# Kernel optimization log

Measured on AMD Instinct MI355X. Metric: run time of the kernel, lower is better.

Reference implementation:

```python
import jax, jax.numpy as jnp
import numpy as np

B, L, D, H = 1024, 128, 768, 256
EPS = 1e-5  # torch BatchNorm1d default eps


def _masked_mean(x, lens):
    # x: [B, L, D], lens: [B] int -> mean over first lens[i] rows per sample
    mask = (jnp.arange(x.shape[1])[None, :] < lens[:, None]).astype(x.dtype)  # [B, L]
    return jnp.einsum('bld,bl->bd', x, mask) / lens[:, None].astype(x.dtype)


def _batchnorm_train(x, gamma, beta):
    # training-mode BN: batch mean and biased variance
    mu = jnp.mean(x, axis=0)
    var = jnp.mean((x - mu) ** 2, axis=0)
    return gamma * (x - mu) / jnp.sqrt(var + EPS) + beta


def setup_inputs() -> dict:
    key = jax.random.key(0)
    ks = jax.random.split(key, 12)
    user_features = jax.random.normal(ks[0], (B, L, D), jnp.float32)
    hashtag_features = jax.random.normal(ks[1], (B, L, D), jnp.float32)
    user_lens = jax.random.randint(ks[2], (B,), 1, L + 1, jnp.int32)
    hashtag_lens = jax.random.randint(ks[3], (B,), 1, L + 1, jnp.int32)
    def lin(k, fan_out, fan_in):
        bound = 1.0 / np.sqrt(fan_in)
        kw, kb = jax.random.split(k)
        w = jax.random.uniform(kw, (fan_out, fan_in), jnp.float32, -bound, bound)
        b = jax.random.uniform(kb, (fan_out,), jnp.float32, -bound, bound)
        return w, b
    fc1_w, fc1_b = lin(ks[4], D, 2 * D)
    fc2_w, fc2_b = lin(ks[5], H, D)
    fc3_w, fc3_b = lin(ks[6], 1, H)
    bn1_g = jnp.ones((D,), jnp.float32)
    bn1_b = jnp.zeros((D,), jnp.float32)
    bn2_g = jnp.ones((H,), jnp.float32)
    bn2_b = jnp.zeros((H,), jnp.float32)
    return {
        'user_features': user_features, 'hashtag_features': hashtag_features,
        'user_lens': user_lens, 'hashtag_lens': hashtag_lens,
        'fc1_w': fc1_w, 'fc1_b': fc1_b, 'bn1_g': bn1_g, 'bn1_b': bn1_b,
        'fc2_w': fc2_w, 'fc2_b': fc2_b, 'bn2_g': bn2_g, 'bn2_b': bn2_b,
        'fc3_w': fc3_w, 'fc3_b': fc3_b,
    }


def reference(user_features, hashtag_features, user_lens, hashtag_lens,
              fc1_w, fc1_b, bn1_g, bn1_b, fc2_w, fc2_b, bn2_g, bn2_b,
              fc3_w, fc3_b):
    # fused ragged mean pooling (replaces per-sample python loop)
    u = _masked_mean(user_features, user_lens)       # [B, D]
    h = _masked_mean(hashtag_features, hashtag_lens)  # [B, D]
    x = jnp.concatenate([u, h], axis=1)               # [B, 2D]
    x = jax.nn.relu(_batchnorm_train(x @ fc1_w.T + fc1_b, bn1_g, bn1_b))
    x = jax.nn.relu(_batchnorm_train(x @ fc2_w.T + fc2_b, bn2_g, bn2_b))
    out = jax.nn.sigmoid(x @ fc3_w.T + fc3_b)          # [B, 1]
    return out
```

## Files before the change

kernel.cpp:

```cpp
#include <hip/hip_runtime.h>
#include <cstdint>
#include <cstddef>

#define BATCH 1024
#define SEQL  128
#define DIM   768
#define HID   256
#define KIN1  1536
#define BN_EPS 1e-5f

typedef unsigned short u16;
typedef __attribute__((ext_vector_type(8))) short short8;
typedef __attribute__((ext_vector_type(4))) float f32x4;

__device__ __forceinline__ u16 f2bf(float f) {
  uint32_t u = __float_as_uint(f);
  return (u16)((u + 0x7fffu + ((u >> 16) & 1u)) >> 16);
}
__device__ __forceinline__ f32x4 ntl(const f32x4* p) { return __builtin_nontemporal_load(p); }
__device__ __forceinline__ float kred(float v) {
  v += __shfl_xor(v, 16);
  v += __shfl_xor(v, 32);
  return v;
}

#define POOL_BLK 4096
#define PREP_BLK 448
#define NW1Q (DIM * KIN1 / 4)
#define NWQ  (NW1Q + HID * DIM / 4)

__global__ __launch_bounds__(96) void pool_prep_kernel(
    const float* __restrict__ uf, const float* __restrict__ hf,
    const int* __restrict__ ul, const int* __restrict__ hl,
    const float* __restrict__ w1, const float* __restrict__ w2,
    u16* __restrict__ xb, u16* __restrict__ w1b, u16* __restrict__ w2b) {
  const int id = blockIdx.x;
  const int t = threadIdx.x;
  if (id < POOL_BLK) {
    const int b = id >> 2;
    const int which = (id >> 1) & 1;
    const int half = id & 1;
    const f32x4* src = (const f32x4*)((which ? hf : uf) + (size_t)b * (SEQL * DIM)) + half * 96;
    const int len = which ? hl[b] : ul[b];
    f32x4 a0 = (f32x4){0.f, 0.f, 0.f, 0.f}, a1 = a0, a2 = a0, a3 = a0;
    int l = 0;
    for (; l + 8 <= len; l += 8) {
      f32x4 v0 = ntl(src + (size_t)(l + 0) * 192 + t);
      f32x4 v1 = ntl(src + (size_t)(l + 1) * 192 + t);
      f32x4 v2 = ntl(src + (size_t)(l + 2) * 192 + t);
      f32x4 v3 = ntl(src + (size_t)(l + 3) * 192 + t);
      f32x4 v4 = ntl(src + (size_t)(l + 4) * 192 + t);
      f32x4 v5 = ntl(src + (size_t)(l + 5) * 192 + t);
      f32x4 v6 = ntl(src + (size_t)(l + 6) * 192 + t);
      f32x4 v7 = ntl(src + (size_t)(l + 7) * 192 + t);
      a0 += v0; a1 += v1; a2 += v2; a3 += v3;
      a0 += v4; a1 += v5; a2 += v6; a3 += v7;
    }
    for (; l < len; ++l) a0 += ntl(src + (size_t)l * 192 + t);
    a0 += a1; a2 += a3; a0 += a2;
    const float s = 1.f / (float)len;
    ushort4 o = make_ushort4(f2bf(a0[0] * s), f2bf(a0[1] * s), f2bf(a0[2] * s), f2bf(a0[3] * s));
    *(ushort4*)(xb + (size_t)b * KIN1 + which * DIM + half * 384 + t * 4) = o;
  } else {
    const int j = id - POOL_BLK;
    const int base = j * 96 + t;
#pragma unroll
    for (int s = 0; s < 8; ++s) {
      const int i = base + s * (PREP_BLK * 96);
      if (i < NW1Q) {
        f32x4 v = ((const f32x4*)w1)[i];
        ((ushort4*)w1b)[i] = make_ushort4(f2bf(v[0]), f2bf(v[1]), f2bf(v[2]), f2bf(v[3]));
      } else {
        const int i2 = i - NW1Q;
        f32x4 v = ((const f32x4*)w2)[i2];
        ((ushort4*)w2b)[i2] = make_ushort4(f2bf(v[0]), f2bf(v[1]), f2bf(v[2]), f2bf(v[3]));
      }
    }
  }
}

#define LDT 72

__global__ __launch_bounds__(256) void gemm1_kernel(
    const u16* __restrict__ A, const u16* __restrict__ W,
    const float* __restrict__ bias, float* __restrict__ y, float* __restrict__ p1) {
  __shared__ u16 lA[2][64 * LDT];
  __shared__ u16 lB[2][64 * LDT];
  __shared__ float red[2][64][2];
  const int K = KIN1, N = DIM;
  const int tid = threadIdx.x, lane = tid & 63, wv = tid >> 6;
  const int wr = wv >> 1, wc = wv & 1;
  const int r16 = lane & 15, kgrp = lane >> 4;
  const int d = blockIdx.x;
  const int g = d & 7, j = d >> 3;
  const int bm = (g >> 1) * 4 + (j & 3);
  const int bn = (g & 1) * 6 + (j >> 2);
  const int sr = tid >> 3, sc8 = (tid & 7) * 8;

  f32x4 acc[2][2];
#pragma unroll
  for (int mi = 0; mi < 2; ++mi)
#pragma unroll
    for (int ni = 0; ni < 2; ++ni) acc[mi][ni] = (f32x4){0.f, 0.f, 0.f, 0.f};

  const u16* Ab = A + (size_t)bm * 64 * K;
  const u16* Wb = W + (size_t)bn * 64 * K;

  uint4 ra0, ra1, rb0, rb1;
#define G1_LOAD(k0)                                              \
  ra0 = *(const uint4*)(Ab + (size_t)sr * K + (k0) + sc8);       \
  ra1 = *(const uint4*)(Ab + (size_t)(sr + 32) * K + (k0) + sc8);\
  rb0 = *(const uint4*)(Wb + (size_t)sr * K + (k0) + sc8);       \
  rb1 = *(const uint4*)(Wb + (size_t)(sr + 32) * K + (k0) + sc8);
#define G1_WRITE(buf)                                \
  *(uint4*)(lA[buf] + sr * LDT + sc8) = ra0;         \
  *(uint4*)(lA[buf] + (sr + 32) * LDT + sc8) = ra1;  \
  *(uint4*)(lB[buf] + sr * LDT + sc8) = rb0;         \
  *(uint4*)(lB[buf] + (sr + 32) * LDT + sc8) = rb1;

  G1_LOAD(0)
  G1_WRITE(0)
  __syncthreads();
  const int nk = K / 64;
  for (int ti = 0; ti < nk; ++ti) {
    const int cur = ti & 1;
    const bool more = (ti + 1 < nk);
    if (more) { G1_LOAD((ti + 1) * 64) }
#pragma unroll
    for (int kk = 0; kk < 2; ++kk) {
      const int koff = (kk * 4 + kgrp) * 8;
      short8 af0 = *(const short8*)(lA[cur] + (wr * 32 + r16) * LDT + koff);
      short8 af1 = *(const short8*)(lA[cur] + (wr * 32 + 16 + r16) * LDT + koff);
      short8 bf0 = *(const short8*)(lB[cur] + (wc * 32 + r16) * LDT + koff);
      short8 bf1 = *(const short8*)(lB[cur] + (wc * 32 + 16 + r16) * LDT + koff);
      acc[0][0] = __builtin_amdgcn_mfma_f32_16x16x32_bf16(af0, bf0, acc[0][0], 0, 0, 0);
      acc[0][1] = __builtin_amdgcn_mfma_f32_16x16x32_bf16(af0, bf1, acc[0][1], 0, 0, 0);
      acc[1][0] = __builtin_amdgcn_mfma_f32_16x16x32_bf16(af1, bf0, acc[1][0], 0, 0, 0);
      acc[1][1] = __builtin_amdgcn_mfma_f32_16x16x32_bf16(af1, bf1, acc[1][1], 0, 0, 0);
    }
    if (more) { G1_WRITE(cur ^ 1) }
    __syncthreads();
  }

#pragma unroll
  for (int ni = 0; ni < 2; ++ni) {
    const int col = bn * 64 + wc * 32 + ni * 16 + r16;
    const float bv = bias[col];
    float s = 0.f, s2 = 0.f;
#pragma unroll
    for (int mi = 0; mi < 2; ++mi)
#pragma unroll
      for (int rg = 0; rg < 4; ++rg) {
        const int row = bm * 64 + wr * 32 + mi * 16 + kgrp * 4 + rg;
        const float v = acc[mi][ni][rg] + bv;
        y[(size_t)row * N + col] = v;
        s += v; s2 += v * v;
      }
    s = kred(s); s2 = kred(s2);
    if (lane < 16) {
      red[wr][wc * 32 + ni * 16 + r16][0] = s;
      red[wr][wc * 32 + ni * 16 + r16][1] = s2;
    }
  }
  __syncthreads();
  if (tid < 128) {
    const int col = tid >> 1, wh = tid & 1;
    p1[((size_t)bm * DIM + bn * 64 + col) * 2 + wh] = red[0][col][wh] + red[1][col][wh];
  }
}

__global__ __launch_bounds__(256) void gemm2_kernel(
    const float* __restrict__ y1, const u16* __restrict__ W,
    const float* __restrict__ bias, const float* __restrict__ g, const float* __restrict__ be,
    const float* __restrict__ p1, float* __restrict__ y2, float* __restrict__ p2) {
  __shared__ u16 lA[2][32 * LDT];
  __shared__ u16 lB[2][32 * LDT];
  __shared__ float sS[DIM], sH[DIM];
  __shared__ float red[2][32][2];
  const int K = DIM, N = HID;
  const int tid = threadIdx.x, lane = tid & 63, wv = tid >> 6;
  const int wr = wv >> 1, wc = wv & 1;
  const int r16 = lane & 15, kgrp = lane >> 4;
  const int d = blockIdx.x;
  const int g8 = d & 7, j = d >> 3;
  const int bm = g8 * 4 + (j & 3);
  const int bn = j >> 2;
  const int sr = tid >> 3, sc8 = (tid & 7) * 8;

  for (int c = tid; c < DIM; c += 256) {
    float s = 0.f, s2 = 0.f;
#pragma unroll
    for (int i = 0; i < 16; ++i) {
      float2 pv = *(const float2*)(p1 + ((size_t)i * DIM + c) * 2);
      s += pv.x; s2 += pv.y;
    }
    const float m = s * (1.f / BATCH);
    const float var = s2 * (1.f / BATCH) - m * m;
    const float r = rsqrtf(var + BN_EPS);
    const float scl = r * g[c];
    sS[c] = scl;
    sH[c] = be[c] - m * scl;
  }
  __syncthreads();

  f32x4 acc = (f32x4){0.f, 0.f, 0.f, 0.f};
  const float* Ab = y1 + (size_t)bm * 32 * K;
  const u16* Wb = W + (size_t)bn * 32 * K;

  f32x4 va0, va1;
  uint4 rbq;
#define G2_LOAD(k0)                                          \
  va0 = *(const f32x4*)(Ab + (size_t)sr * K + (k0) + sc8);   \
  va1 = *(const f32x4*)(Ab + (size_t)sr * K + (k0) + sc8 + 4);\
  rbq = *(const uint4*)(Wb + (size_t)sr * K + (k0) + sc8);

  auto pack_write = [&](int buf, int k0) {
    union { ushort us[8]; uint4 q; } pk;
#pragma unroll
    for (int jj = 0; jj < 4; ++jj) {
      pk.us[jj]     = f2bf(fmaxf(0.f, va0[jj] * sS[k0 + sc8 + jj] + sH[k0 + sc8 + jj]));
      pk.us[4 + jj] = f2bf(fmaxf(0.f, va1[jj] * sS[k0 + sc8 + 4 + jj] + sH[k0 + sc8 + 4 + jj]));
    }
    *(uint4*)(lA[buf] + sr * LDT + sc8) = pk.q;
    *(uint4*)(lB[buf] + sr * LDT + sc8) = rbq;
  };

  G2_LOAD(0)
  pack_write(0, 0);
  __syncthreads();
  const int nk = K / 64;
  for (int ti = 0; ti < nk; ++ti) {
    const int cur = ti & 1;
    const bool more = (ti + 1 < nk);
    if (more) { G2_LOAD((ti + 1) * 64) }
#pragma unroll
    for (int kk = 0; kk < 2; ++kk) {
      const int koff = (kk * 4 + kgrp) * 8;
      short8 af0 = *(const short8*)(lA[cur] + (wr * 16 + r16) * LDT + koff);
      short8 bf0 = *(const short8*)(lB[cur] + (wc * 16 + r16) * LDT + koff);
      acc = __builtin_amdgcn_mfma_f32_16x16x32_bf16(af0, bf0, acc, 0, 0, 0);
    }
    if (more) pack_write(cur ^ 1, (ti + 1) * 64);
    __syncthreads();
  }

  {
    const int col = bn * 32 + wc * 16 + r16;
    const float bv = bias[col];
    float s = 0.f, s2 = 0.f;
#pragma unroll
    for (int rg = 0; rg < 4; ++rg) {
      const int row = bm * 32 + wr * 16 + kgrp * 4 + rg;
      const float v = acc[rg] + bv;
      y2[(size_t)row * N + col] = v;
      s += v; s2 += v * v;
    }
    s = kred(s); s2 = kred(s2);
    if (lane < 16) {
      red[wr][wc * 16 + r16][0] = s;
      red[wr][wc * 16 + r16][1] = s2;
    }
  }
  __syncthreads();
  if (tid < 64) {
    const int col = tid >> 1, wh = tid & 1;
    p2[((size_t)bm * HID + bn * 32 + col) * 2 + wh] = red[0][col][wh] + red[1][col][wh];
  }
}

__global__ __launch_bounds__(256) void fc3_kernel(
    const float* __restrict__ y2, const float* __restrict__ p2,
    const float* __restrict__ g, const float* __restrict__ be,
    const float* __restrict__ w3, const float* __restrict__ b3, float* __restrict__ out) {
  __shared__ float sS[HID], sH[HID];
  const int tid = threadIdx.x;
  {
    const int c = tid;
    float s = 0.f, s2 = 0.f;
#pragma unroll
    for (int i = 0; i < 32; ++i) {
      float2 pv = *(const float2*)(p2 + ((size_t)i * HID + c) * 2);
      s += pv.x; s2 += pv.y;
    }
    const float m = s * (1.f / BATCH);
    const float var = s2 * (1.f / BATCH) - m * m;
    const float r = rsqrtf(var + BN_EPS);
    const float scl = r * g[c];
    sS[c] = scl;
    sH[c] = be[c] - m * scl;
  }
  __syncthreads();
  const int row = blockIdx.x * 4 + (tid >> 6);
  const int lane = tid & 63;
  f32x4 xv = *(const f32x4*)(y2 + (size_t)row * HID + lane * 4);
  f32x4 sc = *(const f32x4*)&sS[lane * 4];
  f32x4 sh = *(const f32x4*)&sH[lane * 4];
  f32x4 wv = *(const f32x4*)(w3 + lane * 4);
  float dsum = 0.f;
#pragma unroll
  for (int jj = 0; jj < 4; ++jj) dsum += fmaxf(0.f, xv[jj] * sc[jj] + sh[jj]) * wv[jj];
#pragma unroll
  for (int off = 32; off > 0; off >>= 1) dsum += __shfl_xor(dsum, off);
  if (lane == 0) out[row] = 1.f / (1.f + expf(-(dsum + b3[0])));
}

extern "C" void kernel_launch(void* const* d_in, const int* in_sizes, int n_in,
                              void* d_out, int out_size, void* d_ws, size_t ws_size,
                              hipStream_t stream) {
  const float* uf   = (const float*)d_in[0];
  const float* hf   = (const float*)d_in[1];
  const int*   ul   = (const int*)d_in[2];
  const int*   hl   = (const int*)d_in[3];
  const float* fc1w = (const float*)d_in[4];
  const float* fc1b = (const float*)d_in[5];
  const float* bn1g = (const float*)d_in[6];
  const float* bn1b = (const float*)d_in[7];
  const float* fc2w = (const float*)d_in[8];
  const float* fc2b = (const float*)d_in[9];
  const float* bn2g = (const float*)d_in[10];
  const float* bn2b = (const float*)d_in[11];
  const float* fc3w = (const float*)d_in[12];
  const float* fc3b = (const float*)d_in[13];
  float* out = (float*)d_out;

  char* ws = (char*)d_ws;
  u16*   xb  = (u16*)  (ws + 0);
  u16*   w1b = (u16*)  (ws + 3145728);
  u16*   w2b = (u16*)  (ws + 5505024);
  float* y1  = (float*)(ws + 5898240);
  float* y2  = (float*)(ws + 9043968);
  float* p1  = (float*)(ws + 10092544);
  float* p2  = (float*)(ws + 10190848);

  pool_prep_kernel<<<POOL_BLK + PREP_BLK, 96, 0, stream>>>(uf, hf, ul, hl, fc1w, fc2w, xb, w1b, w2b);
  gemm1_kernel<<<192, 256, 0, stream>>>(xb, w1b, fc1b, y1, p1);
  gemm2_kernel<<<256, 256, 0, stream>>>(y1, w2b, fc2b, bn1g, bn1b, p1, y2, p2);
  fc3_kernel<<<256, 256, 0, stream>>>(y2, p2, bn2g, bn2b, fc3w, fc3b, out);
}
```

Baseline: 109.8 us.

## Shrink GEMM1 tiles to 32x32 and split pooling into 64-thread thirds

```diff
diff --git a/kernel.cpp b/kernel.cpp
--- a/kernel.cpp
+++ b/kernel.cpp
@@ -17,19 +17,18 @@
   uint32_t u = __float_as_uint(f);
   return (u16)((u + 0x7fffu + ((u >> 16) & 1u)) >> 16);
 }
-__device__ __forceinline__ f32x4 ntl(const f32x4* p) { return __builtin_nontemporal_load(p); }
 __device__ __forceinline__ float kred(float v) {
   v += __shfl_xor(v, 16);
   v += __shfl_xor(v, 32);
   return v;
 }
 
-#define POOL_BLK 4096
-#define PREP_BLK 448
+#define POOL_BLK 6144
+#define PREP_BLK 672
 #define NW1Q (DIM * KIN1 / 4)
 #define NWQ  (NW1Q + HID * DIM / 4)
 
-__global__ __launch_bounds__(96) void pool_prep_kernel(
+__global__ __launch_bounds__(64) void pool_prep_kernel(
     const float* __restrict__ uf, const float* __restrict__ hf,
     const int* __restrict__ ul, const int* __restrict__ hl,
     const float* __restrict__ w1, const float* __restrict__ w2,
@@ -37,36 +36,39 @@
   const int id = blockIdx.x;
   const int t = threadIdx.x;
   if (id < POOL_BLK) {
-    const int b = id >> 2;
-    const int which = (id >> 1) & 1;
-    const int half = id & 1;
-    const f32x4* src = (const f32x4*)((which ? hf : uf) + (size_t)b * (SEQL * DIM)) + half * 96;
-    const int len = which ? hl[b] : ul[b];
+    const int b = id / 6;
+    const int r = id - b * 6;
+    const int which = r >> 1;
+    const int wh2 = r / 3;
+    const int third = r - wh2 * 3;
+    const f32x4* src = (const f32x4*)((wh2 ? hf : uf) + (size_t)b * (SEQL * DIM)) + third * 64;
+    const int len = wh2 ? hl[b] : ul[b];
+    (void)which;
     f32x4 a0 = (f32x4){0.f, 0.f, 0.f, 0.f}, a1 = a0, a2 = a0, a3 = a0;
     int l = 0;
     for (; l + 8 <= len; l += 8) {
-      f32x4 v0 = ntl(src + (size_t)(l + 0) * 192 + t);
-      f32x4 v1 = ntl(src + (size_t)(l + 1) * 192 + t);
-      f32x4 v2 = ntl(src + (size_t)(l + 2) * 192 + t);
-      f32x4 v3 = ntl(src + (size_t)(l + 3) * 192 + t);
-      f32x4 v4 = ntl(src + (size_t)(l + 4) * 192 + t);
-      f32x4 v5 = ntl(src + (size_t)(l + 5) * 192 + t);
-      f32x4 v6 = ntl(src + (size_t)(l + 6) * 192 + t);
-      f32x4 v7 = ntl(src + (size_t)(l + 7) * 192 + t);
+      f32x4 v0 = src[(size_t)(l + 0) * 192 + t];
+      f32x4 v1 = src[(size_t)(l + 1) * 192 + t];
+      f32x4 v2 = src[(size_t)(l + 2) * 192 + t];
+      f32x4 v3 = src[(size_t)(l + 3) * 192 + t];
+      f32x4 v4 = src[(size_t)(l + 4) * 192 + t];
+      f32x4 v5 = src[(size_t)(l + 5) * 192 + t];
+      f32x4 v6 = src[(size_t)(l + 6) * 192 + t];
+      f32x4 v7 = src[(size_t)(l + 7) * 192 + t];
       a0 += v0; a1 += v1; a2 += v2; a3 += v3;
       a0 += v4; a1 += v5; a2 += v6; a3 += v7;
     }
-    for (; l < len; ++l) a0 += ntl(src + (size_t)l * 192 + t);
+    for (; l < len; ++l) a0 += src[(size_t)l * 192 + t];
     a0 += a1; a2 += a3; a0 += a2;
     const float s = 1.f / (float)len;
     ushort4 o = make_ushort4(f2bf(a0[0] * s), f2bf(a0[1] * s), f2bf(a0[2] * s), f2bf(a0[3] * s));
-    *(ushort4*)(xb + (size_t)b * KIN1 + which * DIM + half * 384 + t * 4) = o;
+    *(ushort4*)(xb + (size_t)b * KIN1 + wh2 * DIM + third * 256 + t * 4) = o;
   } else {
     const int j = id - POOL_BLK;
-    const int base = j * 96 + t;
+    const int base = j * 64 + t;
 #pragma unroll
     for (int s = 0; s < 8; ++s) {
-      const int i = base + s * (PREP_BLK * 96);
+      const int i = base + s * (PREP_BLK * 64);
       if (i < NW1Q) {
         f32x4 v = ((const f32x4*)w1)[i];
         ((ushort4*)w1b)[i] = make_ushort4(f2bf(v[0]), f2bf(v[1]), f2bf(v[2]), f2bf(v[3]));
@@ -84,39 +86,30 @@
 __global__ __launch_bounds__(256) void gemm1_kernel(
     const u16* __restrict__ A, const u16* __restrict__ W,
     const float* __restrict__ bias, float* __restrict__ y, float* __restrict__ p1) {
-  __shared__ u16 lA[2][64 * LDT];
-  __shared__ u16 lB[2][64 * LDT];
-  __shared__ float red[2][64][2];
+  __shared__ u16 lA[2][32 * LDT];
+  __shared__ u16 lB[2][32 * LDT];
+  __shared__ float red[2][32][2];
   const int K = KIN1, N = DIM;
   const int tid = threadIdx.x, lane = tid & 63, wv = tid >> 6;
   const int wr = wv >> 1, wc = wv & 1;
   const int r16 = lane & 15, kgrp = lane >> 4;
   const int d = blockIdx.x;
   const int g = d & 7, j = d >> 3;
-  const int bm = (g >> 1) * 4 + (j & 3);
-  const int bn = (g & 1) * 6 + (j >> 2);
+  const int bm = g * 4 + (j & 3);
+  const int bn = j >> 2;
   const int sr = tid >> 3, sc8 = (tid & 7) * 8;
 
-  f32x4 acc[2][2];
-#pragma unroll
-  for (int mi = 0; mi < 2; ++mi)
-#pragma unroll
-    for (int ni = 0; ni < 2; ++ni) acc[mi][ni] = (f32x4){0.f, 0.f, 0.f, 0.f};
-
-  const u16* Ab = A + (size_t)bm * 64 * K;
-  const u16* Wb = W + (size_t)bn * 64 * K;
-
-  uint4 ra0, ra1, rb0, rb1;
-#define G1_LOAD(k0)                                              \
-  ra0 = *(const uint4*)(Ab + (size_t)sr * K + (k0) + sc8);       \
-  ra1 = *(const uint4*)(Ab + (size_t)(sr + 32) * K + (k0) + sc8);\
-  rb0 = *(const uint4*)(Wb + (size_t)sr * K + (k0) + sc8);       \
-  rb1 = *(const uint4*)(Wb + (size_t)(sr + 32) * K + (k0) + sc8);
-#define G1_WRITE(buf)                                \
-  *(uint4*)(lA[buf] + sr * LDT + sc8) = ra0;         \
-  *(uint4*)(lA[buf] + (sr + 32) * LDT + sc8) = ra1;  \
-  *(uint4*)(lB[buf] + sr * LDT + sc8) = rb0;         \
-  *(uint4*)(lB[buf] + (sr + 32) * LDT + sc8) = rb1;
+  f32x4 acc = (f32x4){0.f, 0.f, 0.f, 0.f};
+  const u16* Ab = A + (size_t)bm * 32 * K;
+  const u16* Wb = W + (size_t)bn * 32 * K;
+
+  uint4 ra, rb;
+#define G1_LOAD(k0)                                       \
+  ra = *(const uint4*)(Ab + (size_t)sr * K + (k0) + sc8); \
+  rb = *(const uint4*)(Wb + (size_t)sr * K + (k0) + sc8);
+#define G1_WRITE(buf)                         \
+  *(uint4*)(lA[buf] + sr * LDT + sc8) = ra;   \
+  *(uint4*)(lB[buf] + sr * LDT + sc8) = rb;
 
   G1_LOAD(0)
   G1_WRITE(0)
@@ -129,43 +122,37 @@
 #pragma unroll
     for (int kk = 0; kk < 2; ++kk) {
       const int koff = (kk * 4 + kgrp) * 8;
-      short8 af0 = *(const short8*)(lA[cur] + (wr * 32 + r16) * LDT + koff);
-      short8 af1 = *(const short8*)(lA[cur] + (wr * 32 + 16 + r16) * LDT + koff);
-      short8 bf0 = *(const short8*)(lB[cur] + (wc * 32 + r16) * LDT + koff);
-      short8 bf1 = *(const short8*)(lB[cur] + (wc * 32 + 16 + r16) * LDT + koff);
-      acc[0][0] = __builtin_amdgcn_mfma_f32_16x16x32_bf16(af0, bf0, acc[0][0], 0, 0, 0);
-      acc[0][1] = __builtin_amdgcn_mfma_f32_16x16x32_bf16(af0, bf1, acc[0][1], 0, 0, 0);
-      acc[1][0] = __builtin_amdgcn_mfma_f32_16x16x32_bf16(af1, bf0, acc[1][0], 0, 0, 0);
-      acc[1][1] = __builtin_amdgcn_mfma_f32_16x16x32_bf16(af1, bf1, acc[1][1], 0, 0, 0);
+      short8 af0 = *(const short8*)(lA[cur] + (wr * 16 + r16) * LDT + koff);
+      short8 bf0 = *(const short8*)(lB[cur] + (wc * 16 + r16) * LDT + koff);
+      acc = __builtin_amdgcn_mfma_f32_16x16x32_bf16(af0, bf0, acc, 0, 0, 0);
     }
     if (more) { G1_WRITE(cur ^ 1) }
     __syncthreads();
   }
-
-#pragma unroll
-  for (int ni = 0; ni < 2; ++ni) {
-    const int col = bn * 64 + wc * 32 + ni * 16 + r16;
+#undef G1_LOAD
+#undef G1_WRITE
+
+  {
+    const int col = bn * 32 + wc * 16 + r16;
     const float bv = bias[col];
     float s = 0.f, s2 = 0.f;
 #pragma unroll
-    for (int mi = 0; mi < 2; ++mi)
-#pragma unroll
-      for (int rg = 0; rg < 4; ++rg) {
-        const int row = bm * 64 + wr * 32 + mi * 16 + kgrp * 4 + rg;
-        const float v = acc[mi][ni][rg] + bv;
-        y[(size_t)row * N + col] = v;
-        s += v; s2 += v * v;
-      }
+    for (int rg = 0; rg < 4; ++rg) {
+      const int row = bm * 32 + wr * 16 + kgrp * 4 + rg;
+      const float v = acc[rg] + bv;
+      y[(size_t)row * N + col] = v;
+      s += v; s2 += v * v;
+    }
     s = kred(s); s2 = kred(s2);
     if (lane < 16) {
-      red[wr][wc * 32 + ni * 16 + r16][0] = s;
-      red[wr][wc * 32 + ni * 16 + r16][1] = s2;
-    }
-  }
-  __syncthreads();
-  if (tid < 128) {
+      red[wr][wc * 16 + r16][0] = s;
+      red[wr][wc * 16 + r16][1] = s2;
+    }
+  }
+  __syncthreads();
+  if (tid < 64) {
     const int col = tid >> 1, wh = tid & 1;
-    p1[((size_t)bm * DIM + bn * 64 + col) * 2 + wh] = red[0][col][wh] + red[1][col][wh];
+    p1[((size_t)bm * DIM + bn * 32 + col) * 2 + wh] = red[0][col][wh] + red[1][col][wh];
   }
 }
 
@@ -190,7 +177,7 @@
   for (int c = tid; c < DIM; c += 256) {
     float s = 0.f, s2 = 0.f;
 #pragma unroll
-    for (int i = 0; i < 16; ++i) {
+    for (int i = 0; i < 32; ++i) {
       float2 pv = *(const float2*)(p1 + ((size_t)i * DIM + c) * 2);
       s += pv.x; s2 += pv.y;
     }
@@ -243,6 +230,7 @@
     if (more) pack_write(cur ^ 1, (ti + 1) * 64);
     __syncthreads();
   }
+#undef G2_LOAD
 
   {
     const int col = bn * 32 + wc * 16 + r16;
@@ -330,10 +318,10 @@
   float* y1  = (float*)(ws + 5898240);
   float* y2  = (float*)(ws + 9043968);
   float* p1  = (float*)(ws + 10092544);
-  float* p2  = (float*)(ws + 10190848);
-
-  pool_prep_kernel<<<POOL_BLK + PREP_BLK, 96, 0, stream>>>(uf, hf, ul, hl, fc1w, fc2w, xb, w1b, w2b);
-  gemm1_kernel<<<192, 256, 0, stream>>>(xb, w1b, fc1b, y1, p1);
+  float* p2  = (float*)(ws + 10289152);
+
+  pool_prep_kernel<<<POOL_BLK + PREP_BLK, 64, 0, stream>>>(uf, hf, ul, hl, fc1w, fc2w, xb, w1b, w2b);
+  gemm1_kernel<<<768, 256, 0, stream>>>(xb, w1b, fc1b, y1, p1);
   gemm2_kernel<<<256, 256, 0, stream>>>(y1, w2b, fc2b, bn1g, bn1b, p1, y2, p2);
   fc3_kernel<<<256, 256, 0, stream>>>(y2, p2, bn2g, bn2b, fc3w, fc3b, out);
 }
```

New measurement: 118.3 us. +7.7%, slower.
